# Optimization experiments

Measured on AMD Instinct MI355X. Metric: run time of the kernel, lower is better.

## Reference

```python
import jax, jax.numpy as jnp
import numpy as np

# dims: B batch, R seq_num (MSA rows), L seq_len (residues), D emb_dim, C n_emb_2D, H heads
B, R, L, D, C, H = 1, 256, 384, 512, 256, 4
HD = D // H
SCALE = np.float32((HD ** -0.5) / np.sqrt(L))  # head-dim scaling * seqlen_scaling (1/sqrt(L))
EPS = 1e-5


def setup_inputs() -> dict:
    key = jax.random.key(0)
    ks = jax.random.split(key, 6)
    s = 0.02
    return {
        "x": jax.random.normal(ks[0], (B, R, L, D), jnp.float32),
        "pair_feat": jax.random.normal(ks[1], (B, L, L, C), jnp.float32),
        "attn_mask": jnp.ones((B, L), jnp.int32),
        "ln_msa_g": jnp.ones((D,), jnp.float32),
        "ln_msa_b": jnp.zeros((D,), jnp.float32),
        "ln_pair_g": jnp.ones((C,), jnp.float32),
        "ln_pair_b": jnp.zeros((C,), jnp.float32),
        "W_pair": jax.random.normal(ks[2], (C, H), jnp.float32) * s,  # stacked per-head [C,1] linears
        "W_v": jax.random.normal(ks[3], (D, D), jnp.float32) * s,     # stacked per-head [D,HD] value proj
        "W_out": jax.random.normal(ks[4], (D, D), jnp.float32) * s,   # to_out (bias=False)
    }


def _ln(x, g, b):
    mu = jnp.mean(x, axis=-1, keepdims=True)
    var = jnp.mean(jnp.square(x - mu), axis=-1, keepdims=True)
    return (x - mu) * jax.lax.rsqrt(var + EPS) * g + b


def reference(x, pair_feat, attn_mask, ln_msa_g, ln_msa_b, ln_pair_g, ln_pair_b, W_pair, W_v, W_out):
    # MHPair_to_MSA.forward (eval mode, dropout=0)
    msa = _ln(x, ln_msa_g, ln_msa_b)                                  # [B,R,L,D]
    pf = (pair_feat + jnp.swapaxes(pair_feat, 1, 2)) * 0.5            # symmetrize
    pf = _ln(pf, ln_pair_g, ln_pair_b)                                # [B,L,L,C]
    # pair-feature-derived attention logits (no QK^T)
    logits = jnp.einsum('bijc,ch->bhij', pf * SCALE, W_pair)          # [B,H,L,L]
    V = jnp.einsum('brld,de->brle', msa, W_v).reshape(B, R, L, H, HD) # [B,R,L,H,HD]
    mask2 = attn_mask[:, :, None] * attn_mask[:, None, :]             # [B,L,L]
    logits = jnp.where(mask2[:, None, :, :] == 0,
                       jnp.finfo(logits.dtype).min, logits)
    attn = jax.nn.softmax(logits, axis=-1)                            # [B,H,L,L]
    out = jnp.einsum('bhij,brjhd->brihd', attn, V).reshape(B, R, L, D)
    out = out @ W_out                                                 # to_out, bias=False
    return x + out                                                    # residual
```

## Files before the change

### kernel.cpp

```cpp
#include <hip/hip_runtime.h>

#define L_   384
#define D_   512
#define C_   256
#define H_   4
#define RR_  256
#define M1_  98304
#define LL2_ 147456
#define NPAIR_BLOCKS 18480

typedef __bf16 bf16x8 __attribute__((ext_vector_type(8)));
typedef float f32x4 __attribute__((ext_vector_type(4)));

__device__ __forceinline__ unsigned short f2bf_bits(float f) {
  union { float f; unsigned u; } v; v.f = f;
  return (unsigned short)((v.u + 0x7fffu + ((v.u >> 16) & 1u)) >> 16);
}
__device__ __forceinline__ __bf16 f2bf(float f) {
  union { unsigned short s; __bf16 b; } o; o.s = f2bf_bits(f);
  return o.b;
}

__global__ __launch_bounds__(256) void ln_msa_kernel(
    const float* __restrict__ x, const float* __restrict__ g,
    const float* __restrict__ b, __bf16* __restrict__ msa) {
  int row = blockIdx.x * 4 + (threadIdx.x >> 6);
  int lane = threadIdx.x & 63;
  const float4* xr = (const float4*)(x + (size_t)row * D_ + lane * 8);
  float4 v0 = xr[0], v1 = xr[1];
  float s1 = v0.x + v0.y + v0.z + v0.w + v1.x + v1.y + v1.z + v1.w;
  float s2 = v0.x * v0.x + v0.y * v0.y + v0.z * v0.z + v0.w * v0.w +
             v1.x * v1.x + v1.y * v1.y + v1.z * v1.z + v1.w * v1.w;
#pragma unroll
  for (int o = 32; o > 0; o >>= 1) {
    s1 += __shfl_xor(s1, o);
    s2 += __shfl_xor(s2, o);
  }
  float mu = s1 * (1.0f / D_);
  float var = s2 * (1.0f / D_) - mu * mu;
  float rs = rsqrtf(var + 1e-5f);
  const float4* gp = (const float4*)(g + lane * 8);
  const float4* bp = (const float4*)(b + lane * 8);
  float4 g0 = gp[0], g1 = gp[1], b0 = bp[0], b1 = bp[1];
  float y[8];
  y[0] = (v0.x - mu) * rs * g0.x + b0.x;
  y[1] = (v0.y - mu) * rs * g0.y + b0.y;
  y[2] = (v0.z - mu) * rs * g0.z + b0.z;
  y[3] = (v0.w - mu) * rs * g0.w + b0.w;
  y[4] = (v1.x - mu) * rs * g1.x + b1.x;
  y[5] = (v1.y - mu) * rs * g1.y + b1.y;
  y[6] = (v1.z - mu) * rs * g1.z + b1.z;
  y[7] = (v1.w - mu) * rs * g1.w + b1.w;
  uint4 pk;
  pk.x = ((unsigned)f2bf_bits(y[1]) << 16) | f2bf_bits(y[0]);
  pk.y = ((unsigned)f2bf_bits(y[3]) << 16) | f2bf_bits(y[2]);
  pk.z = ((unsigned)f2bf_bits(y[5]) << 16) | f2bf_bits(y[4]);
  pk.w = ((unsigned)f2bf_bits(y[7]) << 16) | f2bf_bits(y[6]);
  *(uint4*)(msa + (size_t)row * D_ + lane * 8) = pk;
}

__global__ __launch_bounds__(256) void pair_logits_kernel(
    const float* __restrict__ pf, const int* __restrict__ mask,
    const float* __restrict__ g, const float* __restrict__ b,
    const float* __restrict__ Wp, float* __restrict__ logits) {
  unsigned wid = blockIdx.x * 4 + (threadIdx.x >> 6);
  int lane = threadIdx.x & 63;
  unsigned a = wid / 385u;
  unsigned c = wid - a * 385u;
  int i, j;
  if (c < 384u - a) { i = a; j = a + c; }
  else { i = 383 - a; j = i + (c - (384 - a)); }

  int c0 = lane * 4;
  float4 p1 = *(const float4*)(pf + ((size_t)i * L_ + j) * C_ + c0);
  float4 p2 = *(const float4*)(pf + ((size_t)j * L_ + i) * C_ + c0);
  float4 v;
  v.x = 0.5f * (p1.x + p2.x); v.y = 0.5f * (p1.y + p2.y);
  v.z = 0.5f * (p1.z + p2.z); v.w = 0.5f * (p1.w + p2.w);
  float s1 = v.x + v.y + v.z + v.w;
  float s2 = v.x * v.x + v.y * v.y + v.z * v.z + v.w * v.w;
#pragma unroll
  for (int o = 32; o > 0; o >>= 1) {
    s1 += __shfl_xor(s1, o);
    s2 += __shfl_xor(s2, o);
  }
  float mu = s1 * (1.0f / C_);
  float var = s2 * (1.0f / C_) - mu * mu;
  float rs = rsqrtf(var + 1e-5f);
  float4 gv = *(const float4*)(g + c0);
  float4 bv = *(const float4*)(b + c0);
  float y0 = (v.x - mu) * rs * gv.x + bv.x;
  float y1 = (v.y - mu) * rs * gv.y + bv.y;
  float y2 = (v.z - mu) * rs * gv.z + bv.z;
  float y3 = (v.w - mu) * rs * gv.w + bv.w;
  const float4* wp = (const float4*)Wp;
  float4 w0 = wp[c0], w1 = wp[c0 + 1], w2 = wp[c0 + 2], w3 = wp[c0 + 3];
  float4 t;
  t.x = y0 * w0.x + y1 * w1.x + y2 * w2.x + y3 * w3.x;
  t.y = y0 * w0.y + y1 * w1.y + y2 * w2.y + y3 * w3.y;
  t.z = y0 * w0.z + y1 * w1.z + y2 * w2.z + y3 * w3.z;
  t.w = y0 * w0.w + y1 * w1.w + y2 * w2.w + y3 * w3.w;
#pragma unroll
  for (int o = 32; o > 0; o >>= 1) {
    t.x += __shfl_xor(t.x, o);
    t.y += __shfl_xor(t.y, o);
    t.z += __shfl_xor(t.z, o);
    t.w += __shfl_xor(t.w, o);
  }
  if (lane < 8) {
    int h = lane & 3;
    int ii = (lane < 4) ? i : j;
    int jj = (lane < 4) ? j : i;
    bool ok = (mask[i] != 0) && (mask[j] != 0);
    const float NEG = -3.402823466e38f;
    const float SCALE = (float)(0.08838834764831845 / 19.595917942265423);
    float th = (h == 0) ? t.x : (h == 1) ? t.y : (h == 2) ? t.z : t.w;
    logits[(size_t)h * LL2_ + (size_t)ii * L_ + jj] = ok ? SCALE * th : NEG;
  }
}

__global__ __launch_bounds__(256) void softmax_kernel(
    const float* __restrict__ logits, __bf16* __restrict__ attn) {
  int wave = threadIdx.x >> 6, lane = threadIdx.x & 63;
  int row = blockIdx.x * 4 + wave;
  const float* lr = logits + (size_t)row * L_;
  float v[6];
#pragma unroll
  for (int t = 0; t < 6; ++t) v[t] = lr[lane + t * 64];
  float mx = v[0];
#pragma unroll
  for (int t = 1; t < 6; ++t) mx = fmaxf(mx, v[t]);
#pragma unroll
  for (int o = 32; o > 0; o >>= 1) mx = fmaxf(mx, __shfl_xor(mx, o));
  float s = 0.f;
#pragma unroll
  for (int t = 0; t < 6; ++t) { v[t] = __expf(v[t] - mx); s += v[t]; }
#pragma unroll
  for (int o = 32; o > 0; o >>= 1) s += __shfl_xor(s, o);
  float inv = 1.0f / s;
  __bf16* ar = attn + (size_t)row * L_;
#pragma unroll
  for (int t = 0; t < 6; ++t) ar[lane + t * 64] = f2bf(v[t] * inv);
}

__global__ __launch_bounds__(256) void wtrans_kernel(
    const float* __restrict__ Wv, const float* __restrict__ Wo,
    __bf16* __restrict__ WvT, __bf16* __restrict__ WoT) {
  int id = blockIdx.x * 256 + threadIdx.x;
  int m = id >> 18;
  int e = (id >> 9) & 511, d = id & 511;
  const float* W = m ? Wo : Wv;
  __bf16* T = m ? WoT : WvT;
  T[(size_t)e * 512 + d] = f2bf(W[(size_t)d * 512 + e]);
}

__device__ __forceinline__ void gload16(const void* g, void* l) {
  __builtin_amdgcn_global_load_lds(
      (const __attribute__((address_space(1))) void*)g,
      (__attribute__((address_space(3))) void*)l, 16, 0, 0);
}

__device__ __forceinline__ unsigned xcd_swz_3072(unsigned bid) {
  return (bid & 7u) * 384u + (bid >> 3);
}
__device__ __forceinline__ unsigned xcd_swz_768(unsigned bid) {
  return (bid & 7u) * 96u + (bid >> 3);
}

template <int NT>
__device__ __forceinline__ void stage_part32(__bf16* s, const __bf16* g, size_t ld) {
  int tid = threadIdx.x;
#pragma unroll
  for (int i = 0; i < 2; ++i) {
    int cid = i * NT + tid;
    int row = cid >> 2, c = cid & 3;
    int cs = c ^ ((row >> 1) & 3);
    gload16(g + (size_t)row * ld + cs * 8, (char*)s + cid * 16);
  }
}

__device__ __forceinline__ bf16x8 frag_ld32(const __bf16* s, int row, int fk) {
  int c = (fk >> 3) ^ ((row >> 1) & 3);
  return *(const bf16x8*)((const char*)s + row * 64 + c * 16);
}

__device__ __forceinline__ void mainloop256_2s(
    const __bf16* __restrict__ A, size_t ldA,
    const __bf16* __restrict__ B, size_t ldB,
    int K, __bf16* lds, f32x4 acc[8][4]) {
  int lane = threadIdx.x & 63, wave = threadIdx.x >> 6;
  int wm = (wave >> 2) * 128, wn = (wave & 3) * 64;
  int fr = lane & 15, fk = (lane >> 4) * 8;
  int nt = K >> 5;
  const int SLOT = 512 * 32;
  stage_part32<512>(lds, A, ldA);
  stage_part32<512>(lds + 256 * 32, B, ldB);
  for (int t = 0; t < nt; ++t) {
    const __bf16* As = lds + (t & 1) * SLOT;
    const __bf16* Bs = As + 256 * 32;
    if (t + 1 < nt) {
      __bf16* d = lds + ((t + 1) & 1) * SLOT;
      stage_part32<512>(d, A + (size_t)(t + 1) * 32, ldA);
      stage_part32<512>(d + 256 * 32, B + (size_t)(t + 1) * 32, ldB);
      asm volatile("s_waitcnt vmcnt(4)" ::: "memory");
    } else {
      asm volatile("s_waitcnt vmcnt(0)" ::: "memory");
    }
    __builtin_amdgcn_s_barrier();
    bf16x8 bfv[4];
#pragma unroll
    for (int ni = 0; ni < 4; ++ni) bfv[ni] = frag_ld32(Bs, wn + ni * 16 + fr, fk);
#pragma unroll
    for (int half = 0; half < 2; ++half) {
      bf16x8 af[4];
#pragma unroll
      for (int mi = 0; mi < 4; ++mi)
        af[mi] = frag_ld32(As, wm + half * 64 + mi * 16 + fr, fk);
      __builtin_amdgcn_s_setprio(1);
#pragma unroll
      for (int mi = 0; mi < 4; ++mi)
#pragma unroll
        for (int ni = 0; ni < 4; ++ni)
          acc[half * 4 + mi][ni] = __builtin_amdgcn_mfma_f32_16x16x32_bf16(
              af[mi], bfv[ni], acc[half * 4 + mi][ni], 0, 0, 0);
      __builtin_amdgcn_s_setprio(0);
    }
  }
}

__device__ __forceinline__ void mainloop128(
    const __bf16* __restrict__ A, size_t ldA,
    const __bf16* __restrict__ B, size_t ldB,
    int K, __bf16* lds, f32x4 acc[4][4]) {
  int lane = threadIdx.x & 63, wave = threadIdx.x >> 6;
  int wm = (wave >> 1) * 64, wn = (wave & 1) * 64;
  int fr = lane & 15, fk = (lane >> 4) * 8;
  int nt = K >> 5;
  const int SLOT = 256 * 32;
#pragma unroll
  for (int t = 0; t < 3; ++t) {
    stage_part32<256>(lds + t * SLOT, A + t * 32, ldA);
    stage_part32<256>(lds + t * SLOT + 128 * 32, B + t * 32, ldB);
  }
  for (int t = 0; t < nt; ++t) {
    int rem = nt - 1 - t;
    if (rem >= 2)      asm volatile("s_waitcnt vmcnt(8)" ::: "memory");
    else if (rem == 1) asm volatile("s_waitcnt vmcnt(4)" ::: "memory");
    else               asm volatile("s_waitcnt vmcnt(0)" ::: "memory");
    __builtin_amdgcn_s_barrier();
    const __bf16* As = lds + (t & 3) * SLOT;
    const __bf16* Bs = As + 128 * 32;
    if (t + 3 < nt) {
      __bf16* d = lds + ((t + 3) & 3) * SLOT;
      stage_part32<256>(d, A + (size_t)(t + 3) * 32, ldA);
      stage_part32<256>(d + 128 * 32, B + (size_t)(t + 3) * 32, ldB);
    }
    bf16x8 bfv[4];
#pragma unroll
    for (int ni = 0; ni < 4; ++ni) bfv[ni] = frag_ld32(Bs, wn + ni * 16 + fr, fk);
#pragma unroll
    for (int half = 0; half < 2; ++half) {
      bf16x8 af[2];
#pragma unroll
      for (int mi = 0; mi < 2; ++mi)
        af[mi] = frag_ld32(As, wm + half * 32 + mi * 16 + fr, fk);
      __builtin_amdgcn_s_setprio(1);
#pragma unroll
      for (int mi = 0; mi < 2; ++mi)
#pragma unroll
        for (int ni = 0; ni < 4; ++ni)
          acc[half * 2 + mi][ni] = __builtin_amdgcn_mfma_f32_16x16x32_bf16(
              af[mi], bfv[ni], acc[half * 2 + mi][ni], 0, 0, 0);
      __builtin_amdgcn_s_setprio(0);
    }
  }
}

__global__ __launch_bounds__(512) void gemm_vt_kernel(
    const __bf16* __restrict__ WvT, const __bf16* __restrict__ msa,
    __bf16* __restrict__ VT) {
  __shared__ __bf16 lds[2 * 512 * 32];
  unsigned swz = xcd_swz_768(blockIdx.x + 2 * blockIdx.y);
  int m0 = (swz & 1) * 256;
  int n0 = (swz >> 1) * 256;
  f32x4 acc[8][4] = {};
  mainloop256_2s(WvT + (size_t)m0 * D_, D_, msa + (size_t)n0 * D_, D_, D_, lds, acc);
  int lane = threadIdx.x & 63, wave = threadIdx.x >> 6;
  int wm = (wave >> 2) * 128, wn = (wave & 3) * 64;
  int cr = (lane >> 4) * 4, cc = lane & 15;
#pragma unroll
  for (int mi = 0; mi < 8; ++mi)
#pragma unroll
    for (int ni = 0; ni < 4; ++ni)
#pragma unroll
      for (int rr = 0; rr < 4; ++rr) {
        int row = m0 + wm + mi * 16 + cr + rr;
        int col = n0 + wn + ni * 16 + cc;
        VT[(size_t)row * M1_ + col] = f2bf(acc[mi][ni][rr]);
      }
}

__global__ __launch_bounds__(256) void attnv_kernel(
    const __bf16* __restrict__ attn, const __bf16* __restrict__ VT,
    __bf16* __restrict__ out2) {
  __shared__ __bf16 lds[4 * 256 * 32];
  unsigned swz = xcd_swz_3072(blockIdx.x + 3 * blockIdx.y);
  int it = swz % 3u;
  int rh = swz / 3u;
  int h = rh & 3, r = rh >> 2;
  const __bf16* A = attn + (size_t)h * LL2_ + (size_t)it * 128 * L_;
  const __bf16* Bt = VT + (size_t)(h * 128) * M1_ + (size_t)r * L_;
  f32x4 acc[4][4] = {};
  mainloop128(A, L_, Bt, M1_, L_, lds, acc);
  int lane = threadIdx.x & 63, wave = threadIdx.x >> 6;
  int wm = (wave >> 1) * 64, wn = (wave & 1) * 64;
  int cr = (lane >> 4) * 4, cc = lane & 15;
#pragma unroll
  for (int mi = 0; mi < 4; ++mi)
#pragma unroll
    for (int ni = 0; ni < 4; ++ni)
#pragma unroll
      for (int rr = 0; rr < 4; ++rr) {
        int row_i = it * 128 + wm + mi * 16 + cr + rr;
        int col = h * 128 + wn + ni * 16 + cc;
        out2[((size_t)r * L_ + row_i) * D_ + col] = f2bf(acc[mi][ni][rr]);
      }
}

__global__ __launch_bounds__(512) void gemm_out_kernel(
    const __bf16* __restrict__ out2, const __bf16* __restrict__ WoT,
    const float* __restrict__ x, float* __restrict__ out) {
  __shared__ __bf16 lds[2 * 512 * 32];
  unsigned swz = xcd_swz_768(blockIdx.x + 2 * blockIdx.y);
  int n0 = (swz & 1) * 256;
  int m0 = (swz >> 1) * 256;
  f32x4 acc[8][4] = {};
  mainloop256_2s(out2 + (size_t)m0 * D_, D_, WoT + (size_t)n0 * D_, D_, D_, lds, acc);
  int lane = threadIdx.x & 63, wave = threadIdx.x >> 6;
  int wm = (wave >> 2) * 128, wn = (wave & 3) * 64;
  int cr = (lane >> 4) * 4, cc = lane & 15;
#pragma unroll
  for (int mi = 0; mi < 8; ++mi)
#pragma unroll
    for (int ni = 0; ni < 4; ++ni)
#pragma unroll
      for (int rr = 0; rr < 4; ++rr) {
        int row = m0 + wm + mi * 16 + cr + rr;
        int col = n0 + wn + ni * 16 + cc;
        size_t idx = (size_t)row * D_ + col;
        out[idx] = x[idx] + acc[mi][ni][rr];
      }
}

extern "C" void kernel_launch(void* const* d_in, const int* in_sizes, int n_in,
                              void* d_out, int out_size, void* d_ws, size_t ws_size,
                              hipStream_t stream) {
  const float* x      = (const float*)d_in[0];
  const float* pair   = (const float*)d_in[1];
  const int*   mask   = (const int*)d_in[2];
  const float* g_msa  = (const float*)d_in[3];
  const float* b_msa  = (const float*)d_in[4];
  const float* g_pair = (const float*)d_in[5];
  const float* b_pair = (const float*)d_in[6];
  const float* Wp     = (const float*)d_in[7];
  const float* Wv     = (const float*)d_in[8];
  const float* Wo     = (const float*)d_in[9];
  float* out = (float*)d_out;

  char* p = (char*)d_ws;
  auto alloc = [&](size_t bytes) {
    char* r = p;
    p += (bytes + 255) & ~(size_t)255;
    return r;
  };
  __bf16* msa    = (__bf16*)alloc((size_t)M1_ * D_ * 2);
  __bf16* VT     = (__bf16*)alloc((size_t)D_ * M1_ * 2);
  float*  logits = (float*)alloc((size_t)H_ * LL2_ * 4);
  __bf16* attn   = (__bf16*)alloc((size_t)H_ * LL2_ * 2);
  __bf16* WvT    = (__bf16*)alloc((size_t)512 * 512 * 2);
  __bf16* WoT    = (__bf16*)alloc((size_t)512 * 512 * 2);
  __bf16* out2   = msa;

  wtrans_kernel<<<2048, 256, 0, stream>>>(Wv, Wo, WvT, WoT);
  ln_msa_kernel<<<M1_ / 4, 256, 0, stream>>>(x, g_msa, b_msa, msa);
  gemm_vt_kernel<<<dim3(2, M1_ / 256), 512, 0, stream>>>(WvT, msa, VT);
  pair_logits_kernel<<<NPAIR_BLOCKS, 256, 0, stream>>>(pair, mask, g_pair, b_pair, Wp, logits);
  softmax_kernel<<<(H_ * L_) / 4, 256, 0, stream>>>(logits, attn);
  attnv_kernel<<<dim3(3, RR_ * H_), 256, 0, stream>>>(attn, VT, out2);
  gemm_out_kernel<<<dim3(2, M1_ / 256), 512, 0, stream>>>(out2, WoT, x, out);
}
```

Before: 375.9 us.

## Fuse attention-times-V and output projection into one kernel with LDS-resident intermediate

Merges the attn@V GEMM and the W_out projection plus residual into a single kernel. Each block computes a 128-row tile of per-head attention output into LDS, then immediately multiplies it by the corresponding W_out slice, accumulating across heads in registers. This removes the bf16 out2 round trip through global memory and one kernel launch. In exchange it runs one 512-thread block per CU with a large register accumulator, reads W_out fragments straight from global without LDS staging, and has fewer blocks (768) for parallelism.

```diff
diff --git a/kernel.cpp b/kernel.cpp
--- a/kernel.cpp
+++ b/kernel.cpp
@@ -160,9 +160,6 @@
       (__attribute__((address_space(3))) void*)l, 16, 0, 0);
 }
 
-__device__ __forceinline__ unsigned xcd_swz_3072(unsigned bid) {
-  return (bid & 7u) * 384u + (bid >> 3);
-}
 __device__ __forceinline__ unsigned xcd_swz_768(unsigned bid) {
   return (bid & 7u) * 96u + (bid >> 3);
 }
@@ -228,54 +225,6 @@
   }
 }
 
-__device__ __forceinline__ void mainloop128(
-    const __bf16* __restrict__ A, size_t ldA,
-    const __bf16* __restrict__ B, size_t ldB,
-    int K, __bf16* lds, f32x4 acc[4][4]) {
-  int lane = threadIdx.x & 63, wave = threadIdx.x >> 6;
-  int wm = (wave >> 1) * 64, wn = (wave & 1) * 64;
-  int fr = lane & 15, fk = (lane >> 4) * 8;
-  int nt = K >> 5;
-  const int SLOT = 256 * 32;
-#pragma unroll
-  for (int t = 0; t < 3; ++t) {
-    stage_part32<256>(lds + t * SLOT, A + t * 32, ldA);
-    stage_part32<256>(lds + t * SLOT + 128 * 32, B + t * 32, ldB);
-  }
-  for (int t = 0; t < nt; ++t) {
-    int rem = nt - 1 - t;
-    if (rem >= 2)      asm volatile("s_waitcnt vmcnt(8)" ::: "memory");
-    else if (rem == 1) asm volatile("s_waitcnt vmcnt(4)" ::: "memory");
-    else               asm volatile("s_waitcnt vmcnt(0)" ::: "memory");
-    __builtin_amdgcn_s_barrier();
-    const __bf16* As = lds + (t & 3) * SLOT;
-    const __bf16* Bs = As + 128 * 32;
-    if (t + 3 < nt) {
-      __bf16* d = lds + ((t + 3) & 3) * SLOT;
-      stage_part32<256>(d, A + (size_t)(t + 3) * 32, ldA);
-      stage_part32<256>(d + 128 * 32, B + (size_t)(t + 3) * 32, ldB);
-    }
-    bf16x8 bfv[4];
-#pragma unroll
-    for (int ni = 0; ni < 4; ++ni) bfv[ni] = frag_ld32(Bs, wn + ni * 16 + fr, fk);
-#pragma unroll
-    for (int half = 0; half < 2; ++half) {
-      bf16x8 af[2];
-#pragma unroll
-      for (int mi = 0; mi < 2; ++mi)
-        af[mi] = frag_ld32(As, wm + half * 32 + mi * 16 + fr, fk);
-      __builtin_amdgcn_s_setprio(1);
-#pragma unroll
-      for (int mi = 0; mi < 2; ++mi)
-#pragma unroll
-        for (int ni = 0; ni < 4; ++ni)
-          acc[half * 2 + mi][ni] = __builtin_amdgcn_mfma_f32_16x16x32_bf16(
-              af[mi], bfv[ni], acc[half * 2 + mi][ni], 0, 0, 0);
-      __builtin_amdgcn_s_setprio(0);
-    }
-  }
-}
-
 __global__ __launch_bounds__(512) void gemm_vt_kernel(
     const __bf16* __restrict__ WvT, const __bf16* __restrict__ msa,
     __bf16* __restrict__ VT) {
@@ -300,55 +249,116 @@
       }
 }
 
-__global__ __launch_bounds__(256) void attnv_kernel(
+__global__ __launch_bounds__(512, 1) void attnout_kernel(
     const __bf16* __restrict__ attn, const __bf16* __restrict__ VT,
-    __bf16* __restrict__ out2) {
-  __shared__ __bf16 lds[4 * 256 * 32];
-  unsigned swz = xcd_swz_3072(blockIdx.x + 3 * blockIdx.y);
+    const __bf16* __restrict__ WoT, const float* __restrict__ x,
+    float* __restrict__ out) {
+  __shared__ char lds[98304];
+  char* Pl = lds + 65536;
+  unsigned swz = xcd_swz_768(blockIdx.x + 3 * blockIdx.y);
   int it = swz % 3u;
-  int rh = swz / 3u;
-  int h = rh & 3, r = rh >> 2;
-  const __bf16* A = attn + (size_t)h * LL2_ + (size_t)it * 128 * L_;
-  const __bf16* Bt = VT + (size_t)(h * 128) * M1_ + (size_t)r * L_;
-  f32x4 acc[4][4] = {};
-  mainloop128(A, L_, Bt, M1_, L_, lds, acc);
-  int lane = threadIdx.x & 63, wave = threadIdx.x >> 6;
-  int wm = (wave >> 1) * 64, wn = (wave & 1) * 64;
+  int r  = swz / 3u;
+  int tid = threadIdx.x, lane = tid & 63, wave = tid >> 6;
+  int fr = lane & 15, fk = (lane >> 4) * 8;
   int cr = (lane >> 4) * 4, cc = lane & 15;
+  int wi = (wave >> 2) * 64;
+  int we = (wave & 3) * 32;
+  int wf = (wave & 3) * 128;
+
+  f32x4 acc_out[4][8] = {};
+
+  for (int h = 0; h < 4; ++h) {
+    const __bf16* A = attn + (size_t)h * LL2_ + (size_t)(it * 128) * L_;
+    const __bf16* B = VT + (size_t)(h * 128) * M1_ + (size_t)r * L_;
+
+    f32x4 acc_p[4][2] = {};
+    {
+      const int SLOT = 16384;
+      int row = tid >> 2, c = tid & 3;
+      int cs = c ^ ((row >> 1) & 3);
+      auto stageA = [&](int t) {
+        char* d = lds + (t & 3) * SLOT;
+        gload16(A + (size_t)row * L_ + t * 32 + cs * 8, d + tid * 16);
+        gload16(B + (size_t)row * M1_ + t * 32 + cs * 8, d + 8192 + tid * 16);
+      };
+      stageA(0); stageA(1); stageA(2);
+      for (int t = 0; t < 12; ++t) {
+        int rem = 11 - t;
+        if (rem >= 2)      asm volatile("s_waitcnt vmcnt(4)" ::: "memory");
+        else if (rem == 1) asm volatile("s_waitcnt vmcnt(2)" ::: "memory");
+        else               asm volatile("s_waitcnt vmcnt(0)" ::: "memory");
+        __builtin_amdgcn_s_barrier();
+        const __bf16* As = (const __bf16*)(lds + (t & 3) * SLOT);
+        const __bf16* Bs = (const __bf16*)(lds + (t & 3) * SLOT + 8192);
+        if (t + 3 < 12) stageA(t + 3);
+        bf16x8 af[4], bf2[2];
+#pragma unroll
+        for (int mi = 0; mi < 4; ++mi) af[mi] = frag_ld32(As, wi + mi * 16 + fr, fk);
+#pragma unroll
+        for (int ni = 0; ni < 2; ++ni) bf2[ni] = frag_ld32(Bs, we + ni * 16 + fr, fk);
+        __builtin_amdgcn_s_setprio(1);
+#pragma unroll
+        for (int mi = 0; mi < 4; ++mi)
+#pragma unroll
+          for (int ni = 0; ni < 2; ++ni)
+            acc_p[mi][ni] = __builtin_amdgcn_mfma_f32_16x16x32_bf16(
+                af[mi], bf2[ni], acc_p[mi][ni], 0, 0, 0);
+        __builtin_amdgcn_s_setprio(0);
+      }
+    }
+
+#pragma unroll
+    for (int mi = 0; mi < 4; ++mi)
+#pragma unroll
+      for (int ni = 0; ni < 2; ++ni)
+#pragma unroll
+        for (int rr = 0; rr < 4; ++rr) {
+          int il = wi + mi * 16 + cr + rr;
+          int el = we + ni * 16 + cc;
+          *(__bf16*)(Pl + il * 256 + (((el >> 3) ^ (il & 7)) << 4) + (el & 7) * 2) =
+              f2bf(acc_p[mi][ni][rr]);
+        }
+    __syncthreads();
+
+#pragma unroll
+    for (int kk = 0; kk < 4; ++kk) {
+      int e0 = kk * 32;
+      bf16x8 pa[4];
+#pragma unroll
+      for (int mi = 0; mi < 4; ++mi) {
+        int row = wi + mi * 16 + fr;
+        int cch = ((e0 + fk) >> 3) ^ (row & 7);
+        pa[mi] = *(const bf16x8*)(Pl + row * 256 + (cch << 4));
+      }
+      bf16x8 wb[8];
+#pragma unroll
+      for (int ni = 0; ni < 8; ++ni) {
+        int f = wf + ni * 16 + fr;
+        wb[ni] = *(const bf16x8*)(WoT + (size_t)f * 512 + h * 128 + e0 + fk);
+      }
+      __builtin_amdgcn_s_setprio(1);
+#pragma unroll
+      for (int mi = 0; mi < 4; ++mi)
+#pragma unroll
+        for (int ni = 0; ni < 8; ++ni)
+          acc_out[mi][ni] = __builtin_amdgcn_mfma_f32_16x16x32_bf16(
+              pa[mi], wb[ni], acc_out[mi][ni], 0, 0, 0);
+      __builtin_amdgcn_s_setprio(0);
+    }
+    __syncthreads();
+  }
+
+  int mrow0 = r * L_ + it * 128 + wi;
 #pragma unroll
   for (int mi = 0; mi < 4; ++mi)
 #pragma unroll
-    for (int ni = 0; ni < 4; ++ni)
+    for (int ni = 0; ni < 8; ++ni)
 #pragma unroll
       for (int rr = 0; rr < 4; ++rr) {
-        int row_i = it * 128 + wm + mi * 16 + cr + rr;
-        int col = h * 128 + wn + ni * 16 + cc;
-        out2[((size_t)r * L_ + row_i) * D_ + col] = f2bf(acc[mi][ni][rr]);
-      }
-}
-
-__global__ __launch_bounds__(512) void gemm_out_kernel(
-    const __bf16* __restrict__ out2, const __bf16* __restrict__ WoT,
-    const float* __restrict__ x, float* __restrict__ out) {
-  __shared__ __bf16 lds[2 * 512 * 32];
-  unsigned swz = xcd_swz_768(blockIdx.x + 2 * blockIdx.y);
-  int n0 = (swz & 1) * 256;
-  int m0 = (swz >> 1) * 256;
-  f32x4 acc[8][4] = {};
-  mainloop256_2s(out2 + (size_t)m0 * D_, D_, WoT + (size_t)n0 * D_, D_, D_, lds, acc);
-  int lane = threadIdx.x & 63, wave = threadIdx.x >> 6;
-  int wm = (wave >> 2) * 128, wn = (wave & 3) * 64;
-  int cr = (lane >> 4) * 4, cc = lane & 15;
-#pragma unroll
-  for (int mi = 0; mi < 8; ++mi)
-#pragma unroll
-    for (int ni = 0; ni < 4; ++ni)
-#pragma unroll
-      for (int rr = 0; rr < 4; ++rr) {
-        int row = m0 + wm + mi * 16 + cr + rr;
-        int col = n0 + wn + ni * 16 + cc;
+        int row = mrow0 + mi * 16 + cr + rr;
+        int col = wf + ni * 16 + cc;
         size_t idx = (size_t)row * D_ + col;
-        out[idx] = x[idx] + acc[mi][ni][rr];
+        out[idx] = x[idx] + acc_out[mi][ni][rr];
       }
 }
 
@@ -379,13 +389,11 @@
   __bf16* attn   = (__bf16*)alloc((size_t)H_ * LL2_ * 2);
   __bf16* WvT    = (__bf16*)alloc((size_t)512 * 512 * 2);
   __bf16* WoT    = (__bf16*)alloc((size_t)512 * 512 * 2);
-  __bf16* out2   = msa;
 
   wtrans_kernel<<<2048, 256, 0, stream>>>(Wv, Wo, WvT, WoT);
   ln_msa_kernel<<<M1_ / 4, 256, 0, stream>>>(x, g_msa, b_msa, msa);
   gemm_vt_kernel<<<dim3(2, M1_ / 256), 512, 0, stream>>>(WvT, msa, VT);
   pair_logits_kernel<<<NPAIR_BLOCKS, 256, 0, stream>>>(pair, mask, g_pair, b_pair, Wp, logits);
   softmax_kernel<<<(H_ * L_) / 4, 256, 0, stream>>>(logits, attn);
-  attnv_kernel<<<dim3(3, RR_ * H_), 256, 0, stream>>>(attn, VT, out2);
-  gemm_out_kernel<<<dim3(2, M1_ / 256), 512, 0, stream>>>(out2, WoT, x, out);
-}
+  attnout_kernel<<<dim3(3, RR_), 512, 0, stream>>>(attn, VT, WoT, x, out);
+}
```

Result: slower. 403.2 us (+7.3%).
